# Kernel optimization log

Measured on AMD Instinct MI355X. Metric: run time of the kernel, lower is better.

Reference implementation:

```python
import jax, jax.numpy as jnp
import numpy as np

N = 50000      # nodes
E = 600000     # edges
H = 128        # hidden_features (= in_features)
ED = 16        # edge_attr_dim
B = 256        # number of graphs in batch
L = 5          # num_layers
OUT = 128      # out_features


def _xavier(key, shape):
    fan_in, fan_out = shape
    a = float(np.sqrt(6.0 / (fan_in + fan_out)))
    return jax.random.uniform(key, shape, jnp.float32, -a, a)


def setup_inputs() -> dict:
    key = jax.random.key(0)
    ks = jax.random.split(key, 32)
    x = jax.random.normal(ks[0], (N, H), jnp.float32)
    edge_index = jax.random.randint(ks[1], (2, E), 0, N, jnp.int32)
    edge_attr = jax.random.normal(ks[2], (E, ED), jnp.float32)
    batch = jnp.sort(jax.random.randint(ks[3], (N,), 0, B, jnp.int32))
    # per-layer parameters, stacked along leading L axis (in=hidden so uniform)
    node_W = jnp.stack([_xavier(jax.random.fold_in(ks[4], i), (H, H)) for i in range(L)])
    edge_W = jnp.stack([_xavier(jax.random.fold_in(ks[5], i), (ED, H)) for i in range(L)])
    mlp1_W = jnp.stack([_xavier(jax.random.fold_in(ks[6], i), (H, H)) for i in range(L)])
    mlp2_W = jnp.stack([_xavier(jax.random.fold_in(ks[7], i), (H, H)) for i in range(L)])
    zb = jnp.zeros((L, H), jnp.float32)
    # virtual-node update MLP (shared across layers) and final classifier
    vn_w0 = _xavier(ks[8], (H, H)); vn_b0 = jnp.zeros((H,), jnp.float32)
    vn_w1 = _xavier(ks[9], (H, H)); vn_b1 = jnp.zeros((H,), jnp.float32)
    fc_W = _xavier(ks[10], (H, OUT)); fc_b = jnp.zeros((OUT,), jnp.float32)
    vn_init = jnp.zeros((1, H), jnp.float32)  # embedding initialized to 0
    return {
        "x": x, "edge_attr": edge_attr,
        "node_W": node_W, "node_b": zb, "edge_W": edge_W, "edge_b": zb,
        "mlp1_W": mlp1_W, "mlp1_b": zb, "mlp2_W": mlp2_W, "mlp2_b": zb,
        "vn_w0": vn_w0, "vn_b0": vn_b0, "vn_w1": vn_w1, "vn_b1": vn_b1,
        "fc_W": fc_W, "fc_b": fc_b, "vn_init": vn_init,
        "edge_index": edge_index, "batch": batch,
    }


def reference(x, edge_attr, node_W, node_b, edge_W, edge_b, mlp1_W, mlp1_b,
              mlp2_W, mlp2_b, vn_w0, vn_b0, vn_w1, vn_b1, fc_W, fc_b,
              vn_init, edge_index, batch):
    src, dst = edge_index[0], edge_index[1]
    # per-graph node counts for mean pooling (guard against empty graphs)
    counts = jnp.maximum(
        jax.ops.segment_sum(jnp.ones((N, 1), x.dtype), batch, num_segments=B), 1.0)
    vn = jnp.broadcast_to(vn_init, (B, H))  # weight.repeat(batch_size, 1)

    def layer(carry, p):
        xc, vn = carry
        nW, nb, eW, eb, m1W, m1b, m2W, m2b = p
        h = xc @ nW + nb + vn[batch]              # node encode + VN broadcast
        ea = edge_attr @ eW + eb                   # edge encode [E,H]
        msg = h[src] + ea                          # gather + add
        agg = jax.ops.segment_sum(msg, dst, num_segments=N)  # scatter-add
        out = jax.nn.relu(agg @ m1W + m1b) @ m2W + m2b        # layer MLP
        xn = jax.nn.relu(out)
        pooled = jax.ops.segment_sum(xn, batch, num_segments=B) / counts
        vn2 = vn + jax.nn.relu(jax.nn.relu(pooled @ vn_w0 + vn_b0) @ vn_w1 + vn_b1)
        return (xn, vn2), None

    (xf, _), _ = jax.lax.scan(
        layer, (x, vn),
        (node_W, node_b, edge_W, edge_b, mlp1_W, mlp1_b, mlp2_W, mlp2_b))
    pooled = jax.ops.segment_sum(xf, batch, num_segments=B) / counts
    return pooled @ fc_W + fc_b
```

## Files before the change

kernel.cpp:

```cpp
#include <hip/hip_runtime.h>

#define NN 50000
#define EE 600000
#define HH 128
#define EDD 16
#define BB 256
#define LL 5
#define NN16 (NN * 16)
#define NSHADOW 8

typedef float f32x4 __attribute__((ext_vector_type(4)));
typedef _Float16 f16x4 __attribute__((ext_vector_type(4)));
typedef _Float16 f16x8 __attribute__((ext_vector_type(8)));

__global__ __launch_bounds__(256) void wprep_k(const float* __restrict__ W,
    _Float16* __restrict__ Wh, _Float16* __restrict__ Wl, int total)
{
    int idx = blockIdx.x * 256 + threadIdx.x;
    if (idx >= total) return;
    int mat = idx >> 14;
    int r = idx & 16383;
    int j = r & 7, lane = (r >> 3) & 63, ks = (r >> 9) & 3, ntw = (r >> 11) & 7;
    int lm = lane & 15, quad = lane >> 4;
    int n = (ntw >> 1) * 32 + (ntw & 1) * 16 + lm;
    int k = ks * 32 + quad * 8 + j;
    float w = W[(mat << 14) + (k << 7) + n];
    _Float16 h = (_Float16)w;
    Wh[idx] = h;
    Wl[idx] = (_Float16)(w - (float)h);
}

__global__ __launch_bounds__(256) void bext_k(const float* __restrict__ eW,
    const float* __restrict__ eb, const float* __restrict__ nb,
    _Float16* __restrict__ BXh, _Float16* __restrict__ BXl)
{
    int idx = blockIdx.x * 256 + threadIdx.x;
    if (idx >= 5 * 8192) return;
    int j = idx & 7, lane = (idx >> 3) & 63, ks = (idx >> 9) & 1, ntw = (idx >> 10) & 7, l = idx >> 13;
    int lm = lane & 15, quad = lane >> 4;
    int n = (ntw >> 1) * 32 + (ntw & 1) * 16 + lm;
    int k = ks * 32 + quad * 8 + j;
    float v = 0.f;
    if (k < 16) v = eW[((size_t)l * 16 + k) * 128 + n];
    else if (k < 32) v = eW[((size_t)l * 16 + (k - 16)) * 128 + n];
    else if (k == 32) v = eb[l * 128 + n] + nb[l * 128 + n];
    _Float16 h = (_Float16)v;
    BXh[idx] = h;
    BXl[idx] = (_Float16)(v - (float)h);
}

__global__ __launch_bounds__(256) void xprep_k(const float* __restrict__ x,
    _Float16* __restrict__ X)
{
    int i = blockIdx.x * 256 + threadIdx.x;
    if (i >= NN * 32) return;
    float4 v = ((const float4*)x)[i];
    f16x4 o;
    o[0] = (_Float16)v.x; o[1] = (_Float16)v.y; o[2] = (_Float16)v.z; o[3] = (_Float16)v.w;
    ((f16x4*)X)[i] = o;
}

__device__ __forceinline__ void stage_A16(const _Float16* __restrict__ Ag, int M, int brow,
    int tid, _Float16* __restrict__ As)
{
    const int r = tid >> 2, cg = tid & 3;
    const int grow = brow + r;
    _Float16* p = As + r * 136 + cg * 32;
    if (grow < M) {
        const f16x8* s = (const f16x8*)(Ag + (size_t)grow * 128 + cg * 32);
#pragma unroll
        for (int i = 0; i < 4; ++i) ((f16x8*)p)[i] = s[i];
    } else {
        f16x8 z = (f16x8)(_Float16)0;
#pragma unroll
        for (int i = 0; i < 4; ++i) ((f16x8*)p)[i] = z;
    }
}

__device__ __forceinline__ void mfma_stage16(
    const _Float16* __restrict__ As,
    const _Float16* __restrict__ Wh, const _Float16* __restrict__ Wl,
    int wn, int lm, int quad, int lane, f32x4 acc[4][2])
{
    f16x8 Bh[2][4], Bl[2][4];
#pragma unroll
    for (int nt = 0; nt < 2; ++nt)
#pragma unroll
        for (int ks = 0; ks < 4; ++ks) {
            int fi = ((((wn * 2 + nt) * 4) + ks) * 64 + lane) * 8;
            Bh[nt][ks] = *(const f16x8*)(Wh + fi);
            Bl[nt][ks] = *(const f16x8*)(Wl + fi);
        }
#pragma unroll
    for (int ks = 0; ks < 4; ++ks) {
        f16x8 a[4];
#pragma unroll
        for (int mt = 0; mt < 4; ++mt) {
            int off = (mt * 16 + lm) * 136 + ks * 32 + quad * 8;
            a[mt] = *(const f16x8*)(As + off);
        }
#pragma unroll
        for (int mt = 0; mt < 4; ++mt)
#pragma unroll
            for (int nt = 0; nt < 2; ++nt) {
                acc[mt][nt] = __builtin_amdgcn_mfma_f32_16x16x32_f16(a[mt], Bh[nt][ks], acc[mt][nt], 0, 0, 0);
                acc[mt][nt] = __builtin_amdgcn_mfma_f32_16x16x32_f16(a[mt], Bl[nt][ks], acc[mt][nt], 0, 0, 0);
            }
    }
}

__device__ __forceinline__ void store_f16(const _Float16* __restrict__ Fo,
    _Float16* __restrict__ out, int M, int brow, int tid)
{
    const int r = tid >> 2, cg = tid & 3;
    const int grow = brow + r;
    if (grow >= M) return;
    const f16x8* src = (const f16x8*)(Fo + r * 136 + cg * 32);
    f16x8* dst = (f16x8*)(out + (size_t)grow * 128 + cg * 32);
#pragma unroll
    for (int i = 0; i < 4; ++i) dst[i] = src[i];
}

__global__ __launch_bounds__(256) void gemm_fused_k(
    const _Float16* __restrict__ AggX, const _Float16* __restrict__ Afix,
    const _Float16* __restrict__ Cfrag, const _Float16* __restrict__ vnB, int usevn,
    const _Float16* __restrict__ WNh, const _Float16* __restrict__ WNl,
    const _Float16* __restrict__ BXh, const _Float16* __restrict__ BXl,
    const _Float16* __restrict__ W1h, const _Float16* __restrict__ W1l, const float* __restrict__ b1,
    const _Float16* __restrict__ W2h, const _Float16* __restrict__ W2l, const float* __restrict__ b2,
    _Float16* __restrict__ X, float* __restrict__ pooled8,
    const int* __restrict__ batch, int M)
{
    __shared__ __align__(16) _Float16 bufA[64 * 136];
    __shared__ __align__(16) _Float16 bufB[64 * 136];
    const int tid = threadIdx.x, brow = blockIdx.x * 64;

    stage_A16(AggX, M, brow, tid, bufA);
    {
        const int r = tid >> 2, cg = tid & 3;
        const int grow = brow + r;
        _Float16* p = bufB + r * 72 + cg * 16;
        if (grow < M) {
            const f16x8* s = (const f16x8*)(Afix + (size_t)grow * 64 + cg * 16);
            ((f16x8*)p)[0] = s[0]; ((f16x8*)p)[1] = s[1];
        } else {
            f16x8 z = (f16x8)(_Float16)0;
            ((f16x8*)p)[0] = z; ((f16x8*)p)[1] = z;
        }
    }
    __syncthreads();

    const int lane = tid & 63, wn = tid >> 6, lm = lane & 15, quad = lane >> 4;
    const int colb = wn * 32 + lm;

    f32x4 acc[4][2];
#pragma unroll
    for (int mt = 0; mt < 4; ++mt) { acc[mt][0] = (f32x4)(0.f); acc[mt][1] = (f32x4)(0.f); }

    mfma_stage16(bufA, WNh, WNl, wn, lm, quad, lane, acc);

#pragma unroll
    for (int ksf = 0; ksf < 2; ++ksf) {
        f16x8 Bh[2], Bl[2];
#pragma unroll
        for (int nt = 0; nt < 2; ++nt) {
            int fi = (((wn * 2 + nt) * 2 + ksf) * 64 + lane) * 8;
            Bh[nt] = *(const f16x8*)(BXh + fi);
            Bl[nt] = *(const f16x8*)(BXl + fi);
        }
#pragma unroll
        for (int mt = 0; mt < 4; ++mt) {
            f16x8 a = *(const f16x8*)(bufB + (mt * 16 + lm) * 72 + ksf * 32 + quad * 8);
#pragma unroll
            for (int nt = 0; nt < 2; ++nt) {
                acc[mt][nt] = __builtin_amdgcn_mfma_f32_16x16x32_f16(a, Bh[nt], acc[mt][nt], 0, 0, 0);
                acc[mt][nt] = __builtin_amdgcn_mfma_f32_16x16x32_f16(a, Bl[nt], acc[mt][nt], 0, 0, 0);
            }
        }
    }

    if (usevn) {
        const _Float16* Cb = Cfrag + (size_t)blockIdx.x * 16384;
#pragma unroll
        for (int ks = 0; ks < 8; ++ks) {
            f16x8 bv[2];
#pragma unroll
            for (int nt = 0; nt < 2; ++nt)
                bv[nt] = *(const f16x8*)(vnB + (((ks * 8 + (wn * 2 + nt)) * 64 + lane) * 8));
#pragma unroll
            for (int mt = 0; mt < 4; ++mt) {
                f16x8 av = *(const f16x8*)(Cb + (((mt * 8 + ks) * 64 + lane) * 8));
                acc[mt][0] = __builtin_amdgcn_mfma_f32_16x16x32_f16(av, bv[0], acc[mt][0], 0, 0, 0);
                acc[mt][1] = __builtin_amdgcn_mfma_f32_16x16x32_f16(av, bv[1], acc[mt][1], 0, 0, 0);
            }
        }
    }
    __syncthreads();

#pragma unroll
    for (int mt = 0; mt < 4; ++mt) {
#pragma unroll
        for (int r = 0; r < 4; ++r) {
            int trow = mt * 16 + quad * 4 + r;
            bufA[trow * 136 + colb]      = (_Float16)acc[mt][0][r];
            bufA[trow * 136 + colb + 16] = (_Float16)acc[mt][1][r];
        }
    }
    __syncthreads();

#pragma unroll
    for (int mt = 0; mt < 4; ++mt) { acc[mt][0] = (f32x4)(0.f); acc[mt][1] = (f32x4)(0.f); }
    mfma_stage16(bufA, W1h, W1l, wn, lm, quad, lane, acc);
    {
        const float c0 = b1[colb], c1 = b1[colb + 16];
#pragma unroll
        for (int mt = 0; mt < 4; ++mt) {
#pragma unroll
            for (int r = 0; r < 4; ++r) {
                int trow = mt * 16 + quad * 4 + r;
                bufB[trow * 136 + colb]      = (_Float16)fmaxf(acc[mt][0][r] + c0, 0.f);
                bufB[trow * 136 + colb + 16] = (_Float16)fmaxf(acc[mt][1][r] + c1, 0.f);
            }
        }
    }
    __syncthreads();

#pragma unroll
    for (int mt = 0; mt < 4; ++mt) { acc[mt][0] = (f32x4)(0.f); acc[mt][1] = (f32x4)(0.f); }
    mfma_stage16(bufB, W2h, W2l, wn, lm, quad, lane, acc);
    {
        const float d0 = b2[colb], d1 = b2[colb + 16];
#pragma unroll
        for (int mt = 0; mt < 4; ++mt) {
#pragma unroll
            for (int r = 0; r < 4; ++r) {
                int trow = mt * 16 + quad * 4 + r;
                bufA[trow * 136 + colb]      = (_Float16)fmaxf(acc[mt][0][r] + d0, 0.f);
                bufA[trow * 136 + colb + 16] = (_Float16)fmaxf(acc[mt][1][r] + d1, 0.f);
            }
        }
    }
    __syncthreads();
    store_f16(bufA, X, M, brow, tid);

    {
        float* pooled = pooled8 + (size_t)(blockIdx.x & (NSHADOW - 1)) * (BB * HH);
        const int c = tid & 127, half = tid >> 7;
        const int row0 = half * 32;
        float sum = 0.f;
        int curg = -1;
        for (int r2 = 0; r2 < 32; ++r2) {
            int grow = brow + row0 + r2;
            if (grow >= M) break;
            int g = batch[grow];
            if (g != curg) {
                if (curg >= 0) atomicAdd(&pooled[curg * 128 + c], sum);
                curg = g; sum = 0.f;
            }
            sum += (float)bufA[(row0 + r2) * 136 + c];
        }
        if (curg >= 0) atomicAdd(&pooled[curg * 128 + c], sum);
    }
}

__global__ __launch_bounds__(256) void gather_k(
    const _Float16* __restrict__ X, const int* __restrict__ rowstart,
    const int* __restrict__ csrc, _Float16* __restrict__ AggX, int n)
{
    const int tid = threadIdx.x;
    const int lane = tid & 15;
    const int node = blockIdx.x * 16 + (tid >> 4);
    if (node >= n) return;
    const int s = rowstart[node], e = rowstart[node + 1];
    const f16x8* X8 = (const f16x8*)X;

    float ax[8];
#pragma unroll
    for (int k = 0; k < 8; ++k) ax[k] = 0.f;

    int p = s;
    for (; p + 4 <= e; p += 4) {
        int s0 = csrc[p], s1 = csrc[p + 1], s2 = csrc[p + 2], s3 = csrc[p + 3];
        f16x8 x0 = X8[(size_t)s0 * 16 + lane];
        f16x8 x1 = X8[(size_t)s1 * 16 + lane];
        f16x8 x2 = X8[(size_t)s2 * 16 + lane];
        f16x8 x3 = X8[(size_t)s3 * 16 + lane];
#pragma unroll
        for (int k = 0; k < 8; ++k)
            ax[k] += ((float)x0[k] + (float)x1[k]) + ((float)x2[k] + (float)x3[k]);
    }
    for (; p < e; ++p) {
        f16x8 x0 = X8[(size_t)csrc[p] * 16 + lane];
#pragma unroll
        for (int k = 0; k < 8; ++k) ax[k] += (float)x0[k];
    }

    f16x8 o;
#pragma unroll
    for (int k = 0; k < 8; ++k) o[k] = (_Float16)ax[k];
    ((f16x8*)AggX)[(size_t)node * 16 + lane] = o;
}

__global__ __launch_bounds__(256) void aggEat_k(
    const float* __restrict__ eattr, const int* __restrict__ dstv,
    float* __restrict__ aggE)
{
    int i = blockIdx.x * 256 + threadIdx.x;
    if (i >= EE * 16) return;
    int e = i >> 4, k = i & 15;
    atomicAdd(&aggE[(size_t)dstv[e] * 16 + k], eattr[i]);
}

__global__ __launch_bounds__(256) void afix_k(
    const float* __restrict__ aggE, const int* __restrict__ rowstart,
    _Float16* __restrict__ Afix, int n)
{
    const int tid = threadIdx.x;
    const int node = blockIdx.x * 64 + (tid >> 2);
    if (node >= n) return;
    const int cg = tid & 3;
    _Float16* dst = Afix + (size_t)node * 64 + cg * 16;
    f16x8 o0 = (f16x8)(_Float16)0, o1 = (f16x8)(_Float16)0;
    if (cg < 2) {
        const float* ae = aggE + (size_t)node * 16;
#pragma unroll
        for (int k = 0; k < 16; ++k) {
            float v = ae[k];
            _Float16 h = (_Float16)v;
            _Float16 out = (cg == 0) ? h : (_Float16)(v - (float)h);
            if (k < 8) o0[k] = out; else o1[k - 8] = out;
        }
    } else if (cg == 2) {
        o0[0] = (_Float16)(float)(rowstart[node + 1] - rowstart[node]);
    }
    ((f16x8*)dst)[0] = o0;
    ((f16x8*)dst)[1] = o1;
}

__global__ void histC_k(const int* __restrict__ dstv, const int* __restrict__ srcv,
                        const int* __restrict__ batch, int* __restrict__ Cint)
{
    int i = blockIdx.x * 256 + threadIdx.x;
    if (i < EE) atomicAdd(&Cint[(size_t)dstv[i] * 256 + batch[srcv[i]]], 1);
}

__global__ __launch_bounds__(256) void cfrag_k(const int* __restrict__ Cint,
                                               _Float16* __restrict__ Cfrag)
{
    const int brow = blockIdx.x * 64;
    const size_t base = (size_t)blockIdx.x * 16384;
    for (int e = threadIdx.x; e < 16384; e += 256) {
        int j = e & 7, lane = (e >> 3) & 63, ks = (e >> 9) & 7, mt = e >> 12;
        int row = brow + mt * 16 + (lane & 15);
        int g = ks * 32 + (lane >> 4) * 8 + j;
        _Float16 v = (_Float16)0;
        if (row < NN) v = (_Float16)(float)Cint[(size_t)row * 256 + g];
        Cfrag[base + e] = v;
    }
}

__global__ __launch_bounds__(128) void vn_update_k(
    float* __restrict__ pooled8, const int* __restrict__ gstart,
    const float* __restrict__ W0, const float* __restrict__ b0,
    const float* __restrict__ W1, const float* __restrict__ b1,
    float* __restrict__ vn, _Float16* __restrict__ vnB)
{
    __shared__ float p[128], q[128];
    const int g = blockIdx.x, t = threadIdx.x;
    float cnt = (float)(gstart[g + 1] - gstart[g]);
    if (cnt < 1.f) cnt = 1.f;
    float sum = 0.f;
#pragma unroll
    for (int s = 0; s < NSHADOW; ++s) {
        float* slot = pooled8 + (size_t)s * (BB * HH) + g * 128 + t;
        sum += *slot;
        *slot = 0.f;
    }
    p[t] = sum / cnt;
    __syncthreads();
    float a0 = b0[t];
    for (int k = 0; k < 128; ++k) a0 = fmaf(p[k], W0[k * 128 + t], a0);
    q[t] = fmaxf(a0, 0.f);
    __syncthreads();
    float a1 = b1[t];
    for (int k = 0; k < 128; ++k) a1 = fmaf(q[k], W1[k * 128 + t], a1);
    float nv = vn[g * 128 + t] + fmaxf(a1, 0.f);
    vn[g * 128 + t] = nv;
    {
        int ks = g >> 5, quad = (g >> 3) & 3, j = g & 7;
        int tt = ((t >> 5) << 1) | ((t >> 4) & 1);
        int lanev = quad * 16 + (t & 15);
        vnB[((ks * 8 + tt) * 64 + lanev) * 8 + j] = (_Float16)nv;
    }
}

__global__ __launch_bounds__(128) void fc_k(
    const float* __restrict__ pooled8, const int* __restrict__ gstart,
    const float* __restrict__ W, const float* __restrict__ b,
    float* __restrict__ out)
{
    __shared__ float p[128];
    const int g = blockIdx.x, t = threadIdx.x;
    float cnt = (float)(gstart[g + 1] - gstart[g]);
    if (cnt < 1.f) cnt = 1.f;
    float sum = 0.f;
#pragma unroll
    for (int s = 0; s < NSHADOW; ++s)
        sum += pooled8[(size_t)s * (BB * HH) + g * 128 + t];
    p[t] = sum / cnt;
    __syncthreads();
    float acc = b[t];
    for (int k = 0; k < 128; ++k) acc = fmaf(p[k], W[k * 128 + t], acc);
    out[g * 128 + t] = acc;
}

__global__ void histp_k(const int* __restrict__ idx, int n, int* __restrict__ cntp)
{
    int i = blockIdx.x * 256 + threadIdx.x;
    if (i < n) atomicAdd(&cntp[(blockIdx.x & 3) * NN16 + (idx[i] << 4)], 1);
}

__global__ void scan_deg_k(const int* __restrict__ degp, int n, int* __restrict__ out, int* __restrict__ bsum)
{
    __shared__ int s[256];
    int gid = blockIdx.x * 256 + threadIdx.x;
    int v = 0;
    if (gid < n) {
        int o = gid << 4;
        v = degp[o] + degp[NN16 + o] + degp[2 * NN16 + o] + degp[3 * NN16 + o];
    }
    s[threadIdx.x] = v;
    __syncthreads();
    for (int off = 1; off < 256; off <<= 1) {
        int t = (threadIdx.x >= off) ? s[threadIdx.x - off] : 0;
        __syncthreads();
        s[threadIdx.x] += t;
        __syncthreads();
    }
    int incl = s[threadIdx.x];
    if (gid < n) out[gid] = incl - v;
    if (bsum != nullptr && threadIdx.x == 255) bsum[blockIdx.x] = incl;
}

__global__ void scan_k(const int* __restrict__ in, int n, int* __restrict__ out, int* __restrict__ bsum)
{
    __shared__ int s[256];
    int gid = blockIdx.x * 256 + threadIdx.x;
    int v = (gid < n) ? in[gid] : 0;
    s[threadIdx.x] = v;
    __syncthreads();
    for (int off = 1; off < 256; off <<= 1) {
        int t = (threadIdx.x >= off) ? s[threadIdx.x - off] : 0;
        __syncthreads();
        s[threadIdx.x] += t;
        __syncthreads();
    }
    int incl = s[threadIdx.x];
    if (gid < n) out[gid] = incl - v;
    if (bsum != nullptr && threadIdx.x == 255) bsum[blockIdx.x] = incl;
}

__global__ void addoff_k(int* __restrict__ data, const int* __restrict__ boff,
                         int* __restrict__ cursorp, int n, int total)
{
    int i = blockIdx.x * 256 + threadIdx.x;
    if (i < n) {
        int v = data[i] + boff[blockIdx.x];
        data[i] = v;
        cursorp[i << 4] = v;
    }
    if (i == 0) data[n] = total;
}

__global__ void fill_k(const int* __restrict__ dst, const int* __restrict__ src, int n,
                       int* __restrict__ cursorp, int* __restrict__ csrc)
{
    int e = blockIdx.x * 256 + threadIdx.x;
    if (e < n) {
        int slot = atomicAdd(&cursorp[dst[e] << 4], 1);
        csrc[slot] = src[e];
    }
}

__global__ void gstart_k(const int* __restrict__ batch, int* __restrict__ gstart)
{
    int b = blockIdx.x * 64 + threadIdx.x;
    if (b > BB) return;
    if (b == BB) { gstart[BB] = NN; return; }
    int lo = 0, hi = NN;
    while (lo < hi) {
        int mid = (lo + hi) >> 1;
        if (batch[mid] < b) lo = mid + 1; else hi = mid;
    }
    gstart[b] = lo;
}

__global__ void vninit_k(const float* __restrict__ vninit, float* __restrict__ vn,
                         _Float16* __restrict__ vnB, float* __restrict__ pooled8)
{
    int i = blockIdx.x * 256 + threadIdx.x;
    if (i < BB * HH) {
        vn[i] = vninit[i & 127];
        vnB[i] = (_Float16)0;
    }
    if (i < NSHADOW * BB * HH) pooled8[i] = 0.f;
}

extern "C" void kernel_launch(void* const* d_in, const int* in_sizes, int n_in,
                              void* d_out, int out_size, void* d_ws, size_t ws_size,
                              hipStream_t stream)
{
    (void)in_sizes; (void)n_in; (void)out_size; (void)ws_size;
    const float* x       = (const float*)d_in[0];
    const float* eattr   = (const float*)d_in[1];
    const float* node_W  = (const float*)d_in[2];
    const float* node_b  = (const float*)d_in[3];
    const float* edge_W  = (const float*)d_in[4];
    const float* edge_b  = (const float*)d_in[5];
    const float* mlp1_W  = (const float*)d_in[6];
    const float* mlp1_b  = (const float*)d_in[7];
    const float* mlp2_W  = (const float*)d_in[8];
    const float* mlp2_b  = (const float*)d_in[9];
    const float* vn_w0   = (const float*)d_in[10];
    const float* vn_b0   = (const float*)d_in[11];
    const float* vn_w1   = (const float*)d_in[12];
    const float* vn_b1   = (const float*)d_in[13];
    const float* fc_W    = (const float*)d_in[14];
    const float* fc_b    = (const float*)d_in[15];
    const float* vn_init = (const float*)d_in[16];
    const int*   eidx    = (const int*)d_in[17];
    const int*   batch   = (const int*)d_in[18];
    const int* srcv = eidx;
    const int* dstv = eidx + EE;

    char* wp = (char*)d_ws;
    auto alloc = [&](size_t bytes) -> void* {
        void* p = (void*)wp;
        wp += (bytes + 255) & ~(size_t)255;
        return p;
    };
    int* degp      = (int*)alloc((size_t)4 * NN16 * 4);
    int* Cint      = (int*)alloc((size_t)NN * BB * 4);
    float* aggE    = (float*)alloc((size_t)NN * EDD * 4);
    const size_t zero_bytes = (size_t)4 * NN16 * 4 + (size_t)NN * BB * 4 + (size_t)NN * EDD * 4;

    _Float16* X0   = (_Float16*)alloc((size_t)NN * HH * 2);
    _Float16* X    = (_Float16*)alloc((size_t)NN * HH * 2);
    _Float16* AggX = (_Float16*)alloc((size_t)NN * HH * 2);
    _Float16* Afix = (_Float16*)alloc((size_t)NN * 64 * 2);
    _Float16* Cfrag= (_Float16*)alloc((size_t)782 * 16384 * 2);
    float* vn      = (float*)alloc((size_t)BB * HH * 4);
    _Float16* vnB  = (_Float16*)alloc((size_t)BB * HH * 2);
    float* pooled8 = (float*)alloc((size_t)NSHADOW * BB * HH * 4);
    int* rowstart  = (int*)alloc((size_t)(NN + 1) * 4);
    int* cursorp   = (int*)alloc((size_t)NN16 * 4);
    int* csrc      = (int*)alloc((size_t)EE * 4);
    int* bsum      = (int*)alloc(256 * 4);
    int* boff      = (int*)alloc(256 * 4);
    int* gstart    = (int*)alloc((size_t)(BB + 1) * 4);
    _Float16* WtN_h = (_Float16*)alloc((size_t)5 * 16384 * 2);
    _Float16* WtN_l = (_Float16*)alloc((size_t)5 * 16384 * 2);
    _Float16* Wt1_h = (_Float16*)alloc((size_t)5 * 16384 * 2);
    _Float16* Wt1_l = (_Float16*)alloc((size_t)5 * 16384 * 2);
    _Float16* Wt2_h = (_Float16*)alloc((size_t)5 * 16384 * 2);
    _Float16* Wt2_l = (_Float16*)alloc((size_t)5 * 16384 * 2);
    _Float16* BXh   = (_Float16*)alloc((size_t)5 * 8192 * 2);
    _Float16* BXl   = (_Float16*)alloc((size_t)5 * 8192 * 2);

    hipMemsetAsync(degp, 0, zero_bytes, stream);

    histp_k<<<(EE + 255) / 256, 256, 0, stream>>>(dstv, EE, degp);
    histC_k<<<(EE + 255) / 256, 256, 0, stream>>>(dstv, srcv, batch, Cint);
    aggEat_k<<<(EE * 16 + 255) / 256, 256, 0, stream>>>(eattr, dstv, aggE);

    const int NB1 = (NN + 255) / 256;
    scan_deg_k<<<NB1, 256, 0, stream>>>(degp, NN, rowstart, bsum);
    scan_k<<<1, 256, 0, stream>>>(bsum, NB1, boff, nullptr);
    addoff_k<<<NB1, 256, 0, stream>>>(rowstart, boff, cursorp, NN, EE);
    fill_k<<<(EE + 255) / 256, 256, 0, stream>>>(dstv, srcv, EE, cursorp, csrc);

    gstart_k<<<5, 64, 0, stream>>>(batch, gstart);

    afix_k<<<(NN + 63) / 64, 256, 0, stream>>>(aggE, rowstart, Afix, NN);
    cfrag_k<<<(NN + 63) / 64, 256, 0, stream>>>(Cint, Cfrag);
    vninit_k<<<(NSHADOW * BB * HH) / 256, 256, 0, stream>>>(vn_init, vn, vnB, pooled8);
    xprep_k<<<(NN * 32 + 255) / 256, 256, 0, stream>>>(x, X0);

    wprep_k<<<(5 * 16384 + 255) / 256, 256, 0, stream>>>(node_W, WtN_h, WtN_l, 5 * 16384);
    wprep_k<<<(5 * 16384 + 255) / 256, 256, 0, stream>>>(mlp1_W, Wt1_h, Wt1_l, 5 * 16384);
    wprep_k<<<(5 * 16384 + 255) / 256, 256, 0, stream>>>(mlp2_W, Wt2_h, Wt2_l, 5 * 16384);
    bext_k<<<(5 * 8192 + 255) / 256, 256, 0, stream>>>(edge_W, edge_b, node_b, BXh, BXl);

    const int GN = (NN + 63) / 64;
    const _Float16* xin = X0;
    for (int l = 0; l < LL; ++l) {
        gather_k<<<(NN + 15) / 16, 256, 0, stream>>>(xin, rowstart, csrc, AggX, NN);
        gemm_fused_k<<<GN, 256, 0, stream>>>(AggX, Afix, Cfrag, vnB, (l > 0) ? 1 : 0,
            WtN_h + (size_t)l * 16384, WtN_l + (size_t)l * 16384,
            BXh + (size_t)l * 8192, BXl + (size_t)l * 8192,
            Wt1_h + (size_t)l * 16384, Wt1_l + (size_t)l * 16384, mlp1_b + (size_t)l * HH,
            Wt2_h + (size_t)l * 16384, Wt2_l + (size_t)l * 16384, mlp2_b + (size_t)l * HH,
            X, pooled8, batch, NN);
        if (l < LL - 1)
            vn_update_k<<<BB, 128, 0, stream>>>(pooled8, gstart, vn_w0, vn_b0, vn_w1, vn_b1, vn, vnB);
        xin = X;
    }
    fc_k<<<BB, 128, 0, stream>>>(pooled8, gstart, fc_W, fc_b, (float*)d_out);
}
```

Measured before the change: 607.9 us.

## Fuse neighbor gather into layer GEMM kernel and consolidate preprocessing kernels

Moves the per-layer CSR neighbor gather into the fused GEMM kernel so aggregated features are built directly in shared memory, removing the AggX round trip through global memory and one launch per layer. Preprocessing is restructured: the degree histogram and graph-count histogram are merged into one kernel that scatters directly into packed fragment layout (16-bit counters in place, then converted to half), replacing a dense NxB int matrix. Edge-attr aggregation now uses a CSR segmented sum instead of float atomics. Several small init and weight-prep kernels are merged into fewer launches, and X is ping-ponged to avoid in-place hazards. The risks are higher register pressure or load imbalance in the fused layer kernel, and 16-bit packed counters, which could overflow for very high per-graph degree.

```diff
diff --git a/kernel.cpp b/kernel.cpp
--- a/kernel.cpp
+++ b/kernel.cpp
@@ -8,72 +8,67 @@
 #define LL 5
 #define NN16 (NN * 16)
 #define NSHADOW 8
+#define GN 782
 
 typedef float f32x4 __attribute__((ext_vector_type(4)));
 typedef _Float16 f16x4 __attribute__((ext_vector_type(4)));
 typedef _Float16 f16x8 __attribute__((ext_vector_type(8)));
 
-__global__ __launch_bounds__(256) void wprep_k(const float* __restrict__ W,
-    _Float16* __restrict__ Wh, _Float16* __restrict__ Wl, int total)
+__global__ __launch_bounds__(256) void wprep_all_k(
+    const float* __restrict__ W0, const float* __restrict__ W1, const float* __restrict__ W2,
+    _Float16* __restrict__ H0, _Float16* __restrict__ L0,
+    _Float16* __restrict__ H1, _Float16* __restrict__ L1,
+    _Float16* __restrict__ H2, _Float16* __restrict__ L2,
+    const float* __restrict__ eW, const float* __restrict__ eb, const float* __restrict__ nb,
+    _Float16* __restrict__ BXh, _Float16* __restrict__ BXl)
 {
     int idx = blockIdx.x * 256 + threadIdx.x;
-    if (idx >= total) return;
-    int mat = idx >> 14;
-    int r = idx & 16383;
-    int j = r & 7, lane = (r >> 3) & 63, ks = (r >> 9) & 3, ntw = (r >> 11) & 7;
-    int lm = lane & 15, quad = lane >> 4;
-    int n = (ntw >> 1) * 32 + (ntw & 1) * 16 + lm;
-    int k = ks * 32 + quad * 8 + j;
-    float w = W[(mat << 14) + (k << 7) + n];
-    _Float16 h = (_Float16)w;
-    Wh[idx] = h;
-    Wl[idx] = (_Float16)(w - (float)h);
-}
-
-__global__ __launch_bounds__(256) void bext_k(const float* __restrict__ eW,
-    const float* __restrict__ eb, const float* __restrict__ nb,
-    _Float16* __restrict__ BXh, _Float16* __restrict__ BXl)
-{
-    int idx = blockIdx.x * 256 + threadIdx.x;
-    if (idx >= 5 * 8192) return;
-    int j = idx & 7, lane = (idx >> 3) & 63, ks = (idx >> 9) & 1, ntw = (idx >> 10) & 7, l = idx >> 13;
-    int lm = lane & 15, quad = lane >> 4;
-    int n = (ntw >> 1) * 32 + (ntw & 1) * 16 + lm;
-    int k = ks * 32 + quad * 8 + j;
-    float v = 0.f;
-    if (k < 16) v = eW[((size_t)l * 16 + k) * 128 + n];
-    else if (k < 32) v = eW[((size_t)l * 16 + (k - 16)) * 128 + n];
-    else if (k == 32) v = eb[l * 128 + n] + nb[l * 128 + n];
-    _Float16 h = (_Float16)v;
-    BXh[idx] = h;
-    BXl[idx] = (_Float16)(v - (float)h);
-}
-
-__global__ __launch_bounds__(256) void xprep_k(const float* __restrict__ x,
-    _Float16* __restrict__ X)
+    if (idx < 3 * 81920) {
+        int seg = idx / 81920, r = idx - seg * 81920;
+        const float* W = (seg == 0) ? W0 : (seg == 1) ? W1 : W2;
+        _Float16* Wh = (seg == 0) ? H0 : (seg == 1) ? H1 : H2;
+        _Float16* Wl = (seg == 0) ? L0 : (seg == 1) ? L1 : L2;
+        int mat = r >> 14;
+        int rr = r & 16383;
+        int j = rr & 7, lane = (rr >> 3) & 63, ks = (rr >> 9) & 3, ntw = (rr >> 11) & 7;
+        int lm = lane & 15, quad = lane >> 4;
+        int n = (ntw >> 1) * 32 + (ntw & 1) * 16 + lm;
+        int k = ks * 32 + quad * 8 + j;
+        float w = W[(mat << 14) + (k << 7) + n];
+        _Float16 h = (_Float16)w;
+        Wh[r] = h;
+        Wl[r] = (_Float16)(w - (float)h);
+    } else {
+        int i2 = idx - 3 * 81920;
+        if (i2 >= 5 * 8192) return;
+        int j = i2 & 7, lane = (i2 >> 3) & 63, ks = (i2 >> 9) & 1, ntw = (i2 >> 10) & 7, l = i2 >> 13;
+        int lm = lane & 15, quad = lane >> 4;
+        int n = (ntw >> 1) * 32 + (ntw & 1) * 16 + lm;
+        int k = ks * 32 + quad * 8 + j;
+        float v = 0.f;
+        if (k < 16) v = eW[((size_t)l * 16 + k) * 128 + n];
+        else if (k < 32) v = eW[((size_t)l * 16 + (k - 16)) * 128 + n];
+        else if (k == 32) v = eb[l * 128 + n] + nb[l * 128 + n];
+        _Float16 h = (_Float16)v;
+        BXh[i2] = h;
+        BXl[i2] = (_Float16)(v - (float)h);
+    }
+}
+
+__global__ __launch_bounds__(256) void misc_k(const float* __restrict__ x, _Float16* __restrict__ X0,
+    const float* __restrict__ vninit, float* __restrict__ vn, _Float16* __restrict__ vnB,
+    float* __restrict__ pooled8)
 {
     int i = blockIdx.x * 256 + threadIdx.x;
-    if (i >= NN * 32) return;
-    float4 v = ((const float4*)x)[i];
-    f16x4 o;
-    o[0] = (_Float16)v.x; o[1] = (_Float16)v.y; o[2] = (_Float16)v.z; o[3] = (_Float16)v.w;
-    ((f16x4*)X)[i] = o;
-}
-
-__device__ __forceinline__ void stage_A16(const _Float16* __restrict__ Ag, int M, int brow,
-    int tid, _Float16* __restrict__ As)
-{
-    const int r = tid >> 2, cg = tid & 3;
-    const int grow = brow + r;
-    _Float16* p = As + r * 136 + cg * 32;
-    if (grow < M) {
-        const f16x8* s = (const f16x8*)(Ag + (size_t)grow * 128 + cg * 32);
-#pragma unroll
-        for (int i = 0; i < 4; ++i) ((f16x8*)p)[i] = s[i];
+    if (i < NN * 32) {
+        float4 v = ((const float4*)x)[i];
+        f16x4 o;
+        o[0] = (_Float16)v.x; o[1] = (_Float16)v.y; o[2] = (_Float16)v.z; o[3] = (_Float16)v.w;
+        ((f16x4*)X0)[i] = o;
     } else {
-        f16x8 z = (f16x8)(_Float16)0;
-#pragma unroll
-        for (int i = 0; i < 4; ++i) ((f16x8*)p)[i] = z;
+        int k = i - NN * 32;
+        if (k < NSHADOW * BB * HH) pooled8[k] = 0.f;
+        if (k < BB * HH) { vn[k] = vninit[k & 127]; vnB[k] = (_Float16)0; }
     }
 }
 
@@ -121,21 +116,22 @@
     for (int i = 0; i < 4; ++i) dst[i] = src[i];
 }
 
-__global__ __launch_bounds__(256) void gemm_fused_k(
-    const _Float16* __restrict__ AggX, const _Float16* __restrict__ Afix,
+__global__ __launch_bounds__(256) void layer_k(
+    const _Float16* __restrict__ Xin,
+    const _Float16* __restrict__ Afix,
     const _Float16* __restrict__ Cfrag, const _Float16* __restrict__ vnB, int usevn,
+    const int* __restrict__ rowstart, const int2* __restrict__ csr,
     const _Float16* __restrict__ WNh, const _Float16* __restrict__ WNl,
     const _Float16* __restrict__ BXh, const _Float16* __restrict__ BXl,
     const _Float16* __restrict__ W1h, const _Float16* __restrict__ W1l, const float* __restrict__ b1,
     const _Float16* __restrict__ W2h, const _Float16* __restrict__ W2l, const float* __restrict__ b2,
-    _Float16* __restrict__ X, float* __restrict__ pooled8,
+    _Float16* __restrict__ Xout, float* __restrict__ pooled8,
     const int* __restrict__ batch, int M)
 {
     __shared__ __align__(16) _Float16 bufA[64 * 136];
     __shared__ __align__(16) _Float16 bufB[64 * 136];
     const int tid = threadIdx.x, brow = blockIdx.x * 64;
 
-    stage_A16(AggX, M, brow, tid, bufA);
     {
         const int r = tid >> 2, cg = tid & 3;
         const int grow = brow + r;
@@ -148,6 +144,41 @@
             ((f16x8*)p)[0] = z; ((f16x8*)p)[1] = z;
         }
     }
+
+    {
+        const int wv = tid >> 6, grp = (tid >> 4) & 3, li = tid & 15;
+        const f16x8* X8 = (const f16x8*)Xin;
+        for (int j = 0; j < 4; ++j) {
+            int rnode = wv * 16 + grp * 4 + j;
+            int node = brow + rnode;
+            f16x8 o = (f16x8)(_Float16)0;
+            if (node < M) {
+                int s = rowstart[node], e = rowstart[node + 1];
+                float ax[8];
+#pragma unroll
+                for (int k = 0; k < 8; ++k) ax[k] = 0.f;
+                int p = s;
+                for (; p + 4 <= e; p += 4) {
+                    int s0 = csr[p].x, s1 = csr[p + 1].x, s2 = csr[p + 2].x, s3 = csr[p + 3].x;
+                    f16x8 x0 = X8[(size_t)s0 * 16 + li];
+                    f16x8 x1 = X8[(size_t)s1 * 16 + li];
+                    f16x8 x2 = X8[(size_t)s2 * 16 + li];
+                    f16x8 x3 = X8[(size_t)s3 * 16 + li];
+#pragma unroll
+                    for (int k = 0; k < 8; ++k)
+                        ax[k] += ((float)x0[k] + (float)x1[k]) + ((float)x2[k] + (float)x3[k]);
+                }
+                for (; p < e; ++p) {
+                    f16x8 x0 = X8[(size_t)csr[p].x * 16 + li];
+#pragma unroll
+                    for (int k = 0; k < 8; ++k) ax[k] += (float)x0[k];
+                }
+#pragma unroll
+                for (int k = 0; k < 8; ++k) o[k] = (_Float16)ax[k];
+            }
+            *(f16x8*)(bufA + rnode * 136 + li * 8) = o;
+        }
+    }
     __syncthreads();
 
     const int lane = tid & 63, wn = tid >> 6, lm = lane & 15, quad = lane >> 4;
@@ -241,7 +272,7 @@
         }
     }
     __syncthreads();
-    store_f16(bufA, X, M, brow, tid);
+    store_f16(bufA, Xout, M, brow, tid);
 
     {
         float* pooled = pooled8 + (size_t)(blockIdx.x & (NSHADOW - 1)) * (BB * HH);
@@ -263,100 +294,51 @@
     }
 }
 
-__global__ __launch_bounds__(256) void gather_k(
-    const _Float16* __restrict__ X, const int* __restrict__ rowstart,
-    const int* __restrict__ csrc, _Float16* __restrict__ AggX, int n)
-{
-    const int tid = threadIdx.x;
-    const int lane = tid & 15;
-    const int node = blockIdx.x * 16 + (tid >> 4);
+__global__ __launch_bounds__(256) void aggfix_k(
+    const float* __restrict__ eattr, const int* __restrict__ rowstart,
+    const int2* __restrict__ csr, _Float16* __restrict__ Afix, int n)
+{
+    const int lane = threadIdx.x & 15;
+    const int node = blockIdx.x * 16 + (threadIdx.x >> 4);
     if (node >= n) return;
     const int s = rowstart[node], e = rowstart[node + 1];
-    const f16x8* X8 = (const f16x8*)X;
-
-    float ax[8];
-#pragma unroll
-    for (int k = 0; k < 8; ++k) ax[k] = 0.f;
-
-    int p = s;
-    for (; p + 4 <= e; p += 4) {
-        int s0 = csrc[p], s1 = csrc[p + 1], s2 = csrc[p + 2], s3 = csrc[p + 3];
-        f16x8 x0 = X8[(size_t)s0 * 16 + lane];
-        f16x8 x1 = X8[(size_t)s1 * 16 + lane];
-        f16x8 x2 = X8[(size_t)s2 * 16 + lane];
-        f16x8 x3 = X8[(size_t)s3 * 16 + lane];
-#pragma unroll
-        for (int k = 0; k < 8; ++k)
-            ax[k] += ((float)x0[k] + (float)x1[k]) + ((float)x2[k] + (float)x3[k]);
-    }
-    for (; p < e; ++p) {
-        f16x8 x0 = X8[(size_t)csrc[p] * 16 + lane];
-#pragma unroll
-        for (int k = 0; k < 8; ++k) ax[k] += (float)x0[k];
-    }
-
-    f16x8 o;
-#pragma unroll
-    for (int k = 0; k < 8; ++k) o[k] = (_Float16)ax[k];
-    ((f16x8*)AggX)[(size_t)node * 16 + lane] = o;
-}
-
-__global__ __launch_bounds__(256) void aggEat_k(
-    const float* __restrict__ eattr, const int* __restrict__ dstv,
-    float* __restrict__ aggE)
+    float acc = 0.f;
+    for (int p = s; p < e; ++p)
+        acc += eattr[(size_t)csr[p].y * 16 + lane];
+    _Float16 hi = (_Float16)acc;
+    _Float16 lo = (_Float16)(acc - (float)hi);
+    _Float16* A = Afix + (size_t)node * 64;
+    A[lane] = hi;
+    A[16 + lane] = lo;
+    A[32 + lane] = (lane == 0) ? (_Float16)(float)(e - s) : (_Float16)0;
+    A[48 + lane] = (_Float16)0;
+}
+
+__global__ void histboth_k(const int* __restrict__ dstv, const int* __restrict__ srcv,
+                           const int* __restrict__ batch,
+                           int* __restrict__ degp, unsigned int* __restrict__ Cpack)
 {
     int i = blockIdx.x * 256 + threadIdx.x;
-    if (i >= EE * 16) return;
-    int e = i >> 4, k = i & 15;
-    atomicAdd(&aggE[(size_t)dstv[e] * 16 + k], eattr[i]);
-}
-
-__global__ __launch_bounds__(256) void afix_k(
-    const float* __restrict__ aggE, const int* __restrict__ rowstart,
-    _Float16* __restrict__ Afix, int n)
-{
-    const int tid = threadIdx.x;
-    const int node = blockIdx.x * 64 + (tid >> 2);
-    if (node >= n) return;
-    const int cg = tid & 3;
-    _Float16* dst = Afix + (size_t)node * 64 + cg * 16;
-    f16x8 o0 = (f16x8)(_Float16)0, o1 = (f16x8)(_Float16)0;
-    if (cg < 2) {
-        const float* ae = aggE + (size_t)node * 16;
-#pragma unroll
-        for (int k = 0; k < 16; ++k) {
-            float v = ae[k];
-            _Float16 h = (_Float16)v;
-            _Float16 out = (cg == 0) ? h : (_Float16)(v - (float)h);
-            if (k < 8) o0[k] = out; else o1[k - 8] = out;
-        }
-    } else if (cg == 2) {
-        o0[0] = (_Float16)(float)(rowstart[node + 1] - rowstart[node]);
-    }
-    ((f16x8*)dst)[0] = o0;
-    ((f16x8*)dst)[1] = o1;
-}
-
-__global__ void histC_k(const int* __restrict__ dstv, const int* __restrict__ srcv,
-                        const int* __restrict__ batch, int* __restrict__ Cint)
+    if (i >= EE) return;
+    int d = dstv[i];
+    atomicAdd(&degp[(blockIdx.x & 3) * NN16 + (d << 4)], 1);
+    int g = batch[srcv[i]];
+    int blk = d >> 6, rib = d & 63, mt = rib >> 4, lm = rib & 15;
+    int ks = g >> 5, quad = (g >> 3) & 3, j = g & 7;
+    size_t e = (size_t)blk * 16384 + (size_t)(((mt * 8 + ks) * 64) + quad * 16 + lm) * 8 + j;
+    atomicAdd(&Cpack[e >> 1], 1u << ((e & 1) * 16));
+}
+
+__global__ __launch_bounds__(256) void ccvt_k(unsigned int* __restrict__ Cpack)
 {
     int i = blockIdx.x * 256 + threadIdx.x;
-    if (i < EE) atomicAdd(&Cint[(size_t)dstv[i] * 256 + batch[srcv[i]]], 1);
-}
-
-__global__ __launch_bounds__(256) void cfrag_k(const int* __restrict__ Cint,
-                                               _Float16* __restrict__ Cfrag)
-{
-    const int brow = blockIdx.x * 64;
-    const size_t base = (size_t)blockIdx.x * 16384;
-    for (int e = threadIdx.x; e < 16384; e += 256) {
-        int j = e & 7, lane = (e >> 3) & 63, ks = (e >> 9) & 7, mt = e >> 12;
-        int row = brow + mt * 16 + (lane & 15);
-        int g = ks * 32 + (lane >> 4) * 8 + j;
-        _Float16 v = (_Float16)0;
-        if (row < NN) v = (_Float16)(float)Cint[(size_t)row * 256 + g];
-        Cfrag[base + e] = v;
-    }
+    if (i >= GN * 16384 / 2) return;
+    unsigned int v = Cpack[i];
+    _Float16 lo = (_Float16)(float)(v & 0xffffu);
+    _Float16 hi = (_Float16)(float)(v >> 16);
+    unsigned short lu = __builtin_bit_cast(unsigned short, lo);
+    unsigned short hu = __builtin_bit_cast(unsigned short, hi);
+    Cpack[i] = (unsigned int)lu | ((unsigned int)hu << 16);
 }
 
 __global__ __launch_bounds__(128) void vn_update_k(
@@ -412,12 +394,6 @@
     float acc = b[t];
     for (int k = 0; k < 128; ++k) acc = fmaf(p[k], W[k * 128 + t], acc);
     out[g * 128 + t] = acc;
-}
-
-__global__ void histp_k(const int* __restrict__ idx, int n, int* __restrict__ cntp)
-{
-    int i = blockIdx.x * 256 + threadIdx.x;
-    if (i < n) atomicAdd(&cntp[(blockIdx.x & 3) * NN16 + (idx[i] << 4)], 1);
 }
 
 __global__ void scan_deg_k(const int* __restrict__ degp, int n, int* __restrict__ out, int* __restrict__ bsum)
@@ -442,11 +418,11 @@
     if (bsum != nullptr && threadIdx.x == 255) bsum[blockIdx.x] = incl;
 }
 
-__global__ void scan_k(const int* __restrict__ in, int n, int* __restrict__ out, int* __restrict__ bsum)
+__global__ void scan_k(const int* __restrict__ in, int n, int* __restrict__ out,
+                       const int* __restrict__ batch, int* __restrict__ gstart)
 {
     __shared__ int s[256];
-    int gid = blockIdx.x * 256 + threadIdx.x;
-    int v = (gid < n) ? in[gid] : 0;
+    int v = (threadIdx.x < n) ? in[threadIdx.x] : 0;
     s[threadIdx.x] = v;
     __syncthreads();
     for (int off = 1; off < 256; off <<= 1) {
@@ -455,9 +431,17 @@
         s[threadIdx.x] += t;
         __syncthreads();
     }
-    int incl = s[threadIdx.x];
-    if (gid < n) out[gid] = incl - v;
-    if (bsum != nullptr && threadIdx.x == 255) bsum[blockIdx.x] = incl;
+    if (threadIdx.x < n) out[threadIdx.x] = s[threadIdx.x] - v;
+    {
+        int b = threadIdx.x;
+        int lo = 0, hi = NN;
+        while (lo < hi) {
+            int mid = (lo + hi) >> 1;
+            if (batch[mid] < b) lo = mid + 1; else hi = mid;
+        }
+        gstart[b] = lo;
+        if (threadIdx.x == 0) gstart[BB] = NN;
+    }
 }
 
 __global__ void addoff_k(int* __restrict__ data, const int* __restrict__ boff,
@@ -473,37 +457,14 @@
 }
 
 __global__ void fill_k(const int* __restrict__ dst, const int* __restrict__ src, int n,
-                       int* __restrict__ cursorp, int* __restrict__ csrc)
+                       int* __restrict__ cursorp, int2* __restrict__ csr)
 {
     int e = blockIdx.x * 256 + threadIdx.x;
     if (e < n) {
         int slot = atomicAdd(&cursorp[dst[e] << 4], 1);
-        csrc[slot] = src[e];
-    }
-}
-
-__global__ void gstart_k(const int* __restrict__ batch, int* __restrict__ gstart)
-{
-    int b = blockIdx.x * 64 + threadIdx.x;
-    if (b > BB) return;
-    if (b == BB) { gstart[BB] = NN; return; }
-    int lo = 0, hi = NN;
-    while (lo < hi) {
-        int mid = (lo + hi) >> 1;
-        if (batch[mid] < b) lo = mid + 1; else hi = mid;
-    }
-    gstart[b] = lo;
-}
-
-__global__ void vninit_k(const float* __restrict__ vninit, float* __restrict__ vn,
-                         _Float16* __restrict__ vnB, float* __restrict__ pooled8)
-{
-    int i = blockIdx.x * 256 + threadIdx.x;
-    if (i < BB * HH) {
-        vn[i] = vninit[i & 127];
-        vnB[i] = (_Float16)0;
-    }
-    if (i < NSHADOW * BB * HH) pooled8[i] = 0.f;
+        int2 pr; pr.x = src[e]; pr.y = e;
+        csr[slot] = pr;
+    }
 }
 
 extern "C" void kernel_launch(void* const* d_in, const int* in_sizes, int n_in,
@@ -539,22 +500,20 @@
         wp += (bytes + 255) & ~(size_t)255;
         return p;
     };
-    int* degp      = (int*)alloc((size_t)4 * NN16 * 4);
-    int* Cint      = (int*)alloc((size_t)NN * BB * 4);
-    float* aggE    = (float*)alloc((size_t)NN * EDD * 4);
-    const size_t zero_bytes = (size_t)4 * NN16 * 4 + (size_t)NN * BB * 4 + (size_t)NN * EDD * 4;
+    int* degp       = (int*)alloc((size_t)4 * NN16 * 4);
+    _Float16* Cfrag = (_Float16*)alloc((size_t)GN * 16384 * 2);
+    const size_t zero_bytes = (size_t)4 * NN16 * 4 + (size_t)GN * 16384 * 2;
 
     _Float16* X0   = (_Float16*)alloc((size_t)NN * HH * 2);
-    _Float16* X    = (_Float16*)alloc((size_t)NN * HH * 2);
-    _Float16* AggX = (_Float16*)alloc((size_t)NN * HH * 2);
+    _Float16* X1   = (_Float16*)alloc((size_t)NN * HH * 2);
+    _Float16* X2   = (_Float16*)alloc((size_t)NN * HH * 2);
     _Float16* Afix = (_Float16*)alloc((size_t)NN * 64 * 2);
-    _Float16* Cfrag= (_Float16*)alloc((size_t)782 * 16384 * 2);
     float* vn      = (float*)alloc((size_t)BB * HH * 4);
     _Float16* vnB  = (_Float16*)alloc((size_t)BB * HH * 2);
     float* pooled8 = (float*)alloc((size_t)NSHADOW * BB * HH * 4);
     int* rowstart  = (int*)alloc((size_t)(NN + 1) * 4);
     int* cursorp   = (int*)alloc((size_t)NN16 * 4);
-    int* csrc      = (int*)alloc((size_t)EE * 4);
+    int2* csr      = (int2*)alloc((size_t)EE * 8);
     int* bsum      = (int*)alloc(256 * 4);
     int* boff      = (int*)alloc(256 * 4);
     int* gstart    = (int*)alloc((size_t)(BB + 1) * 4);
@@ -567,43 +526,36 @@
     _Float16* BXh   = (_Float16*)alloc((size_t)5 * 8192 * 2);
     _Float16* BXl   = (_Float16*)alloc((size_t)5 * 8192 * 2);
 
-    hipMemsetAsync(degp, 0, zero_bytes, stream);
-
-    histp_k<<<(EE + 255) / 256, 256, 0, stream>>>(dstv, EE, degp);
-    histC_k<<<(EE + 255) / 256, 256, 0, stream>>>(dstv, srcv, batch, Cint);
-    aggEat_k<<<(EE * 16 + 255) / 256, 256, 0, stream>>>(eattr, dstv, aggE);
+    (void)hipMemsetAsync(degp, 0, zero_bytes, stream);
+
+    histboth_k<<<(EE + 255) / 256, 256, 0, stream>>>(dstv, srcv, batch, degp, (unsigned int*)Cfrag);
 
     const int NB1 = (NN + 255) / 256;
     scan_deg_k<<<NB1, 256, 0, stream>>>(degp, NN, rowstart, bsum);
-    scan_k<<<1, 256, 0, stream>>>(bsum, NB1, boff, nullptr);
+    scan_k<<<1, 256, 0, stream>>>(bsum, NB1, boff, batch, gstart);
     addoff_k<<<NB1, 256, 0, stream>>>(rowstart, boff, cursorp, NN, EE);
-    fill_k<<<(EE + 255) / 256, 256, 0, stream>>>(dstv, srcv, EE, cursorp, csrc);
-
-    gstart_k<<<5, 64, 0, stream>>>(batch, gstart);
-
-    afix_k<<<(NN + 63) / 64, 256, 0, stream>>>(aggE, rowstart, Afix, NN);
-    cfrag_k<<<(NN + 63) / 64, 256, 0, stream>>>(Cint, Cfrag);
-    vninit_k<<<(NSHADOW * BB * HH) / 256, 256, 0, stream>>>(vn_init, vn, vnB, pooled8);
-    xprep_k<<<(NN * 32 + 255) / 256, 256, 0, stream>>>(x, X0);
-
-    wprep_k<<<(5 * 16384 + 255) / 256, 256, 0, stream>>>(node_W, WtN_h, WtN_l, 5 * 16384);
-    wprep_k<<<(5 * 16384 + 255) / 256, 256, 0, stream>>>(mlp1_W, Wt1_h, Wt1_l, 5 * 16384);
-    wprep_k<<<(5 * 16384 + 255) / 256, 256, 0, stream>>>(mlp2_W, Wt2_h, Wt2_l, 5 * 16384);
-    bext_k<<<(5 * 8192 + 255) / 256, 256, 0, stream>>>(edge_W, edge_b, node_b, BXh, BXl);
-
-    const int GN = (NN + 63) / 64;
+    fill_k<<<(EE + 255) / 256, 256, 0, stream>>>(dstv, srcv, EE, cursorp, csr);
+    aggfix_k<<<(NN + 15) / 16, 256, 0, stream>>>(eattr, rowstart, csr, Afix, NN);
+    ccvt_k<<<(GN * 16384 / 2 + 255) / 256, 256, 0, stream>>>((unsigned int*)Cfrag);
+
+    misc_k<<<(NN * 32 + NSHADOW * BB * HH) / 256, 256, 0, stream>>>(x, X0, vn_init, vn, vnB, pooled8);
+    wprep_all_k<<<(3 * 81920 + 5 * 8192) / 256, 256, 0, stream>>>(
+        node_W, mlp1_W, mlp2_W, WtN_h, WtN_l, Wt1_h, Wt1_l, Wt2_h, Wt2_l,
+        edge_W, edge_b, node_b, BXh, BXl);
+
     const _Float16* xin = X0;
     for (int l = 0; l < LL; ++l) {
-        gather_k<<<(NN + 15) / 16, 256, 0, stream>>>(xin, rowstart, csrc, AggX, NN);
-        gemm_fused_k<<<GN, 256, 0, stream>>>(AggX, Afix, Cfrag, vnB, (l > 0) ? 1 : 0,
+        _Float16* xout = (l & 1) ? X2 : X1;
+        layer_k<<<GN, 256, 0, stream>>>(xin, Afix, Cfrag, vnB, (l > 0) ? 1 : 0,
+            rowstart, csr,
             WtN_h + (size_t)l * 16384, WtN_l + (size_t)l * 16384,
             BXh + (size_t)l * 8192, BXl + (size_t)l * 8192,
             Wt1_h + (size_t)l * 16384, Wt1_l + (size_t)l * 16384, mlp1_b + (size_t)l * HH,
             Wt2_h + (size_t)l * 16384, Wt2_l + (size_t)l * 16384, mlp2_b + (size_t)l * HH,
-            X, pooled8, batch, NN);
+            xout, pooled8, batch, NN);
         if (l < LL - 1)
             vn_update_k<<<BB, 128, 0, stream>>>(pooled8, gstart, vn_w0, vn_b0, vn_w1, vn_b1, vn, vnB);
-        xin = X;
+        xin = xout;
     }
     fc_k<<<BB, 128, 0, stream>>>(pooled8, gstart, fc_W, fc_b, (float*)d_out);
 }
```

Result: faster. 558.6 us (-8.1%).
